# Performance work log

Hardware: AMD Instinct MI355X
Metric: run time of the kernel (lower is better)

## Reference

```python
import jax, jax.numpy as jnp
import numpy as np

B, N, IN_F, OUT_F, H = 4, 1024, 256, 256, 8
HID = OUT_F // H  # 32
ALPHA = 0.2  # leaky relu negative slope


def setup_inputs() -> dict:
    key = jax.random.key(0)
    k1, k2, k3, k4 = jax.random.split(key, 4)
    h = jax.random.normal(k1, (B, N, IN_F), dtype=jnp.float32)
    # linear: in_features -> n_heads*n_hidden, no bias (stored as [in, out])
    W = jax.random.normal(k2, (IN_F, H * HID), dtype=jnp.float32) / np.sqrt(IN_F)
    # attn: Linear(2*n_hidden, 1, bias=False), shared across heads
    attn_w = jax.random.normal(k3, (2 * HID,), dtype=jnp.float32) / np.sqrt(2 * HID)
    # random dense adjacency (p=0.5) plus self loops, broadcast over heads
    u = jax.random.uniform(k4, (B, N, N, 1), dtype=jnp.float32)
    adj_mat = jnp.maximum((u < 0.5).astype(jnp.float32), jnp.eye(N, dtype=jnp.float32)[None, :, :, None])
    return {"h": h, "adj_mat": adj_mat, "W": W, "attn_w": attn_w}


def reference(h, adj_mat, W, attn_w):
    # g: [b, n, h, d]
    g = (h @ W).reshape(B, N, H, HID)
    # attn(concat(g_i, g_j)) decomposes: e[b,i,j,h] = <attn_w[:HID], g_i> + <attn_w[HID:], g_j>
    # (exactly the math of the repeat/repeat_interleave/cat + 1-wide linear, without the N^2 concat)
    e_i = jnp.einsum('bnhd,d->bnh', g, attn_w[:HID])   # g_repeat_interleave part (index i)
    e_j = jnp.einsum('bnhd,d->bnh', g, attn_w[HID:])   # g_repeat part (index j)
    e = e_i[:, :, None, :] + e_j[:, None, :, :]        # [b, i, j, h]
    e = jnp.where(e >= 0, e, ALPHA * e)                # LeakyReLU(alpha)
    e = jnp.where(adj_mat == 0, -jnp.inf, e)           # masked_fill
    a = jax.nn.softmax(e, axis=1)                      # faithful: original uses Softmax(dim=1)
    # dropout p acts as identity in eval mode / p=0
    out = jnp.einsum('bijh,bjhd->bihd', a, g)          # [b, i, h, d]
    return out.reshape(B, N, H * HID)                  # is_concat=True
```

## Files before the change

kernel.cpp:

```cpp
#include <hip/hip_runtime.h>
#include <math.h>

#define BB 4
#define NN 1024
#define HH 8
#define NROW (BB*NN)

typedef short s8v __attribute__((ext_vector_type(8)));
typedef float f4v __attribute__((ext_vector_type(4)));

__device__ __forceinline__ float lrelu(float x) { return fmaxf(x, 0.2f * x); }
__device__ __forceinline__ short bf16rne(float f) {
    unsigned u = __float_as_uint(f);
    u += 0x7FFF + ((u >> 16) & 1u);
    return (short)(u >> 16);
}

__global__ __launch_bounds__(256) void k_gemm_ei(const float* __restrict__ hm,
                                                 const float* __restrict__ W,
                                                 const float* __restrict__ aw,
                                                 float* __restrict__ g,
                                                 float* __restrict__ e_i,
                                                 float* __restrict__ e_j,
                                                 float* __restrict__ e_jt) {
    __shared__ __align__(16) float hs[8][256];
    __shared__ float aws[64];
    const int row0 = blockIdx.x * 8;
    const int t = threadIdx.x;
    if (t < 64) aws[t] = aw[t];
    const float4* h4 = (const float4*)(hm + row0 * 256);
    float4* hs4 = (float4*)&hs[0][0];
    hs4[t] = h4[t];
    hs4[t + 256] = h4[t + 256];
    __syncthreads();

    float c0 = 0.f, c1 = 0.f, c2 = 0.f, c3 = 0.f, c4 = 0.f, c5 = 0.f, c6 = 0.f, c7 = 0.f;
    for (int k4 = 0; k4 < 64; ++k4) {
        const float w0 = W[(4 * k4 + 0) * 256 + t];
        const float w1 = W[(4 * k4 + 1) * 256 + t];
        const float w2 = W[(4 * k4 + 2) * 256 + t];
        const float w3 = W[(4 * k4 + 3) * 256 + t];
#define ROW(r)                                                        \
        {                                                             \
            const float4 hv = *(const float4*)&hs[r][4 * k4];         \
            c##r = fmaf(hv.x, w0, c##r);                              \
            c##r = fmaf(hv.y, w1, c##r);                              \
            c##r = fmaf(hv.z, w2, c##r);                              \
            c##r = fmaf(hv.w, w3, c##r);                              \
        }
        ROW(0) ROW(1) ROW(2) ROW(3) ROW(4) ROW(5) ROW(6) ROW(7)
#undef ROW
    }
    const int d = t & 31, hh = t >> 5;
    const int b = row0 >> 10;
#define EPI(r)                                                                  \
    {                                                                           \
        g[(row0 + r) * 256 + t] = c##r;                                         \
        float vi = c##r * aws[d];                                               \
        float vj = c##r * aws[32 + d];                                          \
        for (int mm = 1; mm < 32; mm <<= 1) {                                   \
            vi += __shfl_xor(vi, mm);                                           \
            vj += __shfl_xor(vj, mm);                                           \
        }                                                                       \
        if (d == 0) {                                                           \
            e_i[(row0 + r) * 8 + hh] = vi;                                      \
            e_j[(row0 + r) * 8 + hh] = vj;                                      \
            e_jt[(size_t)(b * 8 + hh) * NN + ((row0 + r) & (NN - 1))] = vj;     \
        }                                                                       \
    }
    EPI(0) EPI(1) EPI(2) EPI(3) EPI(4) EPI(5) EPI(6) EPI(7)
#undef EPI
}

__global__ __launch_bounds__(256) void k_s(const float* __restrict__ adj,
                                           const float* __restrict__ e_i,
                                           const float* __restrict__ e_j,
                                           float* __restrict__ ps,
                                           unsigned long long* __restrict__ bits) {
    __shared__ __align__(16) float eis[128 * 8];
    __shared__ float ejs[8][64];
    __shared__ float sp[4][8][64];
    const int bx = blockIdx.x;
    const int b = bx >> 7, jc = (bx >> 3) & 15, ic = bx & 7;
    const int j0 = jc * 64, i0 = ic * 128;
    const int t = threadIdx.x;

    ((float4*)eis)[t] = ((const float4*)(e_i + (b * NN + i0) * 8))[t];
    if (t < 128) {
        const float4 v = ((const float4*)(e_j + (b * NN + j0) * 8))[t];
        const int base = t * 4;
        ejs[(base + 0) & 7][(base + 0) >> 3] = v.x;
        ejs[(base + 1) & 7][(base + 1) >> 3] = v.y;
        ejs[(base + 2) & 7][(base + 2) >> 3] = v.z;
        ejs[(base + 3) & 7][(base + 3) >> 3] = v.w;
    }
    __syncthreads();

    const int ii = t >> 6, jj = t & 63;
    const float e0 = ejs[0][jj], e1 = ejs[1][jj], e2 = ejs[2][jj], e3 = ejs[3][jj];
    const float e4 = ejs[4][jj], e5 = ejs[5][jj], e6 = ejs[6][jj], e7 = ejs[7][jj];
    float s0 = 0.f, s1 = 0.f, s2 = 0.f, s3 = 0.f, s4 = 0.f, s5 = 0.f, s6 = 0.f, s7 = 0.f;
    const float* adjp = adj + (size_t)b * NN * NN + j0 + jj;
    for (int i = ii; i < 128; i += 4) {
        const float a = adjp[(size_t)(i0 + i) * NN];
        const unsigned long long mk = __ballot(a != 0.f);
        if (jj == 0) bits[(size_t)(b * NN + i0 + i) * 16 + jc] = mk;
        const f4v eA = *(const f4v*)&eis[i * 8];
        const f4v eB = *(const f4v*)&eis[i * 8 + 4];
        s0 = fmaf(a, __expf(lrelu(eA[0] + e0)), s0);
        s1 = fmaf(a, __expf(lrelu(eA[1] + e1)), s1);
        s2 = fmaf(a, __expf(lrelu(eA[2] + e2)), s2);
        s3 = fmaf(a, __expf(lrelu(eA[3] + e3)), s3);
        s4 = fmaf(a, __expf(lrelu(eB[0] + e4)), s4);
        s5 = fmaf(a, __expf(lrelu(eB[1] + e5)), s5);
        s6 = fmaf(a, __expf(lrelu(eB[2] + e6)), s6);
        s7 = fmaf(a, __expf(lrelu(eB[3] + e7)), s7);
    }
    sp[ii][0][jj] = s0; sp[ii][1][jj] = s1; sp[ii][2][jj] = s2; sp[ii][3][jj] = s3;
    sp[ii][4][jj] = s4; sp[ii][5][jj] = s5; sp[ii][6][jj] = s6; sp[ii][7][jj] = s7;
    __syncthreads();
#pragma unroll
    for (int k = 0; k < 2; ++k) {
        const int idx = t * 2 + k;
        const int jjo = idx >> 3, h = idx & 7;
        const float s = sp[0][h][jjo] + sp[1][h][jjo] + sp[2][h][jjo] + sp[3][h][jjo];
        ps[ic * (NROW * 8) + (b * NN + j0 + jjo) * 8 + h] = s;
    }
}

__global__ __launch_bounds__(256) void k_prep(const float* __restrict__ ps,
                                              const float* __restrict__ g,
                                              short* __restrict__ Gt) {
    __shared__ float rss[16][8];
    const int bx = blockIdx.x;
    const int b = bx >> 6, j0 = (bx & 63) * 16;
    const int t = threadIdx.x;
    if (t < 128) {
        const int jj = t >> 3, h = t & 7;
        float s = 0.f;
#pragma unroll
        for (int ic = 0; ic < 8; ++ic)
            s += ps[ic * (NROW * 8) + (b * NN + j0 + jj) * 8 + h];
        rss[jj][h] = 1.0f / s;
    }
    __syncthreads();
    const int h = t >> 5, d = t & 31;
    uint4 w0, w1;
#define PK(dst, r0, r1)                                                          \
    {                                                                            \
        const float va = g[(size_t)(b * NN + j0 + r0) * 256 + t] * rss[r0][h];   \
        const float vb = g[(size_t)(b * NN + j0 + r1) * 256 + t] * rss[r1][h];   \
        dst = (unsigned)(unsigned short)bf16rne(va) |                            \
              ((unsigned)(unsigned short)bf16rne(vb) << 16);                     \
    }
    PK(w0.x, 0, 1) PK(w0.y, 2, 3) PK(w0.z, 4, 5) PK(w0.w, 6, 7)
    PK(w1.x, 8, 9) PK(w1.y, 10, 11) PK(w1.z, 12, 13) PK(w1.w, 14, 15)
#undef PK
    const int jt = j0 >> 5, jj0 = j0 & 31;
    short* dst = Gt + ((size_t)((b * 8 + h) * 32 + jt)) * 1024 + d * 32 + jj0;
    *(uint4*)dst = w0;
    *(uint4*)(dst + 8) = w1;
}

__global__ __launch_bounds__(256) void k_out_mfma(const unsigned long long* __restrict__ bits,
                                                  const short* __restrict__ Gt,
                                                  const float* __restrict__ e_i,
                                                  const float* __restrict__ e_jt,
                                                  float* __restrict__ out) {
    __shared__ short gts[4][4][32][40];
    __shared__ float ejt[4][128];
    const int bx = blockIdx.x;
    const int hs = bx >> 8, b = (bx >> 6) & 3, i0 = (bx & 63) * 16;
    const int t = threadIdx.x;
    const int wave = t >> 6, lane = t & 63;
    const int m = lane & 15, q = lane >> 4;
    const int h = hs * 4 + wave;

    const float ei = e_i[(size_t)(b * NN + i0 + m) * 8 + h];
    f4v acc0 = {0.f, 0.f, 0.f, 0.f}, acc1 = {0.f, 0.f, 0.f, 0.f};

    const unsigned long long* bitsrow = bits + (size_t)(b * NN + i0 + m) * 16;
    const float4* gtg4 = (const float4*)Gt;
    const float4* ejt4 = (const float4*)(e_jt + (size_t)b * 8 * NN);

    for (int s = 0; s < 8; ++s) {
        float4 g0, g1, g2, g3, g4, g5, g6, g7;
#define LG(k)                                                                     \
        {                                                                         \
            const int u = t + 256 * (k);                                          \
            g##k = gtg4[(size_t)(b * 8 + hs * 4 + (u >> 9)) * 4096 + s * 512 +    \
                        (u & 511)];                                               \
        }
        LG(0) LG(1) LG(2) LG(3) LG(4) LG(5) LG(6) LG(7)
#undef LG
        const ulonglong2 bv = *(const ulonglong2*)&bitsrow[s * 2];
        float4 ev = make_float4(0.f, 0.f, 0.f, 0.f);
        if (t < 128) ev = ejt4[(size_t)(hs * 4 + (t >> 5)) * 256 + s * 32 + (t & 31)];
        __syncthreads();
#define SG(k)                                                                     \
        {                                                                         \
            const int u = t + 256 * (k);                                          \
            char* dstp = (char*)gts + (u >> 9) * 10240 + ((u >> 7) & 3) * 2560 +  \
                         ((u >> 2) & 31) * 80 + (u & 3) * 16;                     \
            *(float4*)dstp = g##k;                                                \
        }
        SG(0) SG(1) SG(2) SG(3) SG(4) SG(5) SG(6) SG(7)
#undef SG
        if (t < 128) *(float4*)&ejt[t >> 5][(t & 31) * 4] = ev;
        __syncthreads();

        const unsigned bw0 = (unsigned)bv.x, bw1 = (unsigned)(bv.x >> 32);
        const unsigned bw2 = (unsigned)bv.y, bw3 = (unsigned)(bv.y >> 32);

#define LT(lt, bw)                                                                \
        {                                                                         \
            const f4v ej0 = *(const f4v*)&ejt[wave][(lt) * 32 + q * 8];           \
            const f4v ej1 = *(const f4v*)&ejt[wave][(lt) * 32 + q * 8 + 4];       \
            s8v A;                                                                \
            A[0] = ((bw >> (q * 8 + 0)) & 1u) ? bf16rne(__expf(lrelu(ei + ej0[0]))) : (short)0; \
            A[1] = ((bw >> (q * 8 + 1)) & 1u) ? bf16rne(__expf(lrelu(ei + ej0[1]))) : (short)0; \
            A[2] = ((bw >> (q * 8 + 2)) & 1u) ? bf16rne(__expf(lrelu(ei + ej0[2]))) : (short)0; \
            A[3] = ((bw >> (q * 8 + 3)) & 1u) ? bf16rne(__expf(lrelu(ei + ej0[3]))) : (short)0; \
            A[4] = ((bw >> (q * 8 + 4)) & 1u) ? bf16rne(__expf(lrelu(ei + ej1[0]))) : (short)0; \
            A[5] = ((bw >> (q * 8 + 5)) & 1u) ? bf16rne(__expf(lrelu(ei + ej1[1]))) : (short)0; \
            A[6] = ((bw >> (q * 8 + 6)) & 1u) ? bf16rne(__expf(lrelu(ei + ej1[2]))) : (short)0; \
            A[7] = ((bw >> (q * 8 + 7)) & 1u) ? bf16rne(__expf(lrelu(ei + ej1[3]))) : (short)0; \
            const s8v B0 = *(const s8v*)&gts[wave][lt][m][q * 8];                 \
            const s8v B1 = *(const s8v*)&gts[wave][lt][m + 16][q * 8];            \
            acc0 = __builtin_amdgcn_mfma_f32_16x16x32_bf16(A, B0, acc0, 0, 0, 0); \
            acc1 = __builtin_amdgcn_mfma_f32_16x16x32_bf16(A, B1, acc1, 0, 0, 0); \
        }
        LT(0, bw0) LT(1, bw1) LT(2, bw2) LT(3, bw3)
#undef LT
    }

    float* op = out + (size_t)(b * NN + i0) * 256;
#pragma unroll
    for (int r = 0; r < 4; ++r) {
        const int row = q * 4 + r;
        op[(size_t)row * 256 + h * 32 + m] = acc0[r];
        op[(size_t)row * 256 + h * 32 + 16 + m] = acc1[r];
    }
}

extern "C" void kernel_launch(void* const* d_in, const int* in_sizes, int n_in,
                              void* d_out, int out_size, void* d_ws, size_t ws_size,
                              hipStream_t stream) {
    const float* h      = (const float*)d_in[0];
    const float* adj    = (const float*)d_in[1];
    const float* W      = (const float*)d_in[2];
    const float* attn_w = (const float*)d_in[3];
    float* out = (float*)d_out;

    float* ws = (float*)d_ws;
    float* g    = ws;
    float* e_i  = g + NROW * 256;
    float* e_j  = e_i + NROW * 8;
    float* e_jt = e_j + NROW * 8;
    float* ps   = e_jt + NROW * 8;
    short* Gt   = (short*)(ps + 8 * NROW * 8);
    unsigned long long* bits = (unsigned long long*)(Gt + 2 * 1048576);

    k_gemm_ei<<<NROW / 8, 256, 0, stream>>>(h, W, attn_w, g, e_i, e_j, e_jt);
    k_s<<<512, 256, 0, stream>>>(adj, e_i, e_j, ps, bits);
    k_prep<<<256, 256, 0, stream>>>(ps, g, Gt);
    k_out_mfma<<<512, 256, 0, stream>>>(bits, Gt, e_i, e_jt, out);
}
```

Before: 129.2 us.

## Split output kernel over j halves with atomic accumulation and use exp2

The final MFMA kernel now splits the j (neighbor) dimension into two halves, doubling the grid to 1024 blocks and accumulating partial results into the output with float atomicAdd after zeroing it with a memset. Separately, the attention logits are prescaled by log2(e) so the exponentials can use the hardware exp2 instruction instead of __expf. The split is meant to add parallelism and occupancy for a kernel whose grid was about two blocks per CU. The cost is an extra memset, atomic traffic on the output, and nondeterministic summation order.

```diff
diff --git a/kernel.cpp b/kernel.cpp
--- a/kernel.cpp
+++ b/kernel.cpp
@@ -5,11 +5,13 @@
 #define NN 1024
 #define HH 8
 #define NROW (BB*NN)
+#define L2E 1.4426950408889634f
 
 typedef short s8v __attribute__((ext_vector_type(8)));
 typedef float f4v __attribute__((ext_vector_type(4)));
 
 __device__ __forceinline__ float lrelu(float x) { return fmaxf(x, 0.2f * x); }
+__device__ __forceinline__ float fexp2(float x) { return __builtin_amdgcn_exp2f(x); }
 __device__ __forceinline__ short bf16rne(float f) {
     unsigned u = __float_as_uint(f);
     u += 0x7FFF + ((u >> 16) & 1u);
@@ -63,9 +65,9 @@
             vj += __shfl_xor(vj, mm);                                           \
         }                                                                       \
         if (d == 0) {                                                           \
-            e_i[(row0 + r) * 8 + hh] = vi;                                      \
-            e_j[(row0 + r) * 8 + hh] = vj;                                      \
-            e_jt[(size_t)(b * 8 + hh) * NN + ((row0 + r) & (NN - 1))] = vj;     \
+            e_i[(row0 + r) * 8 + hh] = vi * L2E;                                \
+            e_j[(row0 + r) * 8 + hh] = vj * L2E;                                \
+            e_jt[(size_t)(b * 8 + hh) * NN + ((row0 + r) & (NN - 1))] = vj * L2E; \
         }                                                                       \
     }
     EPI(0) EPI(1) EPI(2) EPI(3) EPI(4) EPI(5) EPI(6) EPI(7)
@@ -107,14 +109,14 @@
         if (jj == 0) bits[(size_t)(b * NN + i0 + i) * 16 + jc] = mk;
         const f4v eA = *(const f4v*)&eis[i * 8];
         const f4v eB = *(const f4v*)&eis[i * 8 + 4];
-        s0 = fmaf(a, __expf(lrelu(eA[0] + e0)), s0);
-        s1 = fmaf(a, __expf(lrelu(eA[1] + e1)), s1);
-        s2 = fmaf(a, __expf(lrelu(eA[2] + e2)), s2);
-        s3 = fmaf(a, __expf(lrelu(eA[3] + e3)), s3);
-        s4 = fmaf(a, __expf(lrelu(eB[0] + e4)), s4);
-        s5 = fmaf(a, __expf(lrelu(eB[1] + e5)), s5);
-        s6 = fmaf(a, __expf(lrelu(eB[2] + e6)), s6);
-        s7 = fmaf(a, __expf(lrelu(eB[3] + e7)), s7);
+        s0 = fmaf(a, fexp2(lrelu(eA[0] + e0)), s0);
+        s1 = fmaf(a, fexp2(lrelu(eA[1] + e1)), s1);
+        s2 = fmaf(a, fexp2(lrelu(eA[2] + e2)), s2);
+        s3 = fmaf(a, fexp2(lrelu(eA[3] + e3)), s3);
+        s4 = fmaf(a, fexp2(lrelu(eB[0] + e4)), s4);
+        s5 = fmaf(a, fexp2(lrelu(eB[1] + e5)), s5);
+        s6 = fmaf(a, fexp2(lrelu(eB[2] + e6)), s6);
+        s7 = fmaf(a, fexp2(lrelu(eB[3] + e7)), s7);
     }
     sp[ii][0][jj] = s0; sp[ii][1][jj] = s1; sp[ii][2][jj] = s2; sp[ii][3][jj] = s3;
     sp[ii][4][jj] = s4; sp[ii][5][jj] = s5; sp[ii][6][jj] = s6; sp[ii][7][jj] = s7;
@@ -167,10 +169,10 @@
                                                   const float* __restrict__ e_i,
                                                   const float* __restrict__ e_jt,
                                                   float* __restrict__ out) {
-    __shared__ short gts[4][4][32][40];
-    __shared__ float ejt[4][128];
+    __shared__ short gts[4][2][32][40];
+    __shared__ float ejt[4][64];
     const int bx = blockIdx.x;
-    const int hs = bx >> 8, b = (bx >> 6) & 3, i0 = (bx & 63) * 16;
+    const int jhalf = bx >> 9, hs = (bx >> 8) & 1, b = (bx >> 6) & 3, i0 = (bx & 63) * 16;
     const int t = threadIdx.x;
     const int wave = t >> 6, lane = t & 63;
     const int m = lane & 15, q = lane >> 4;
@@ -179,58 +181,58 @@
     const float ei = e_i[(size_t)(b * NN + i0 + m) * 8 + h];
     f4v acc0 = {0.f, 0.f, 0.f, 0.f}, acc1 = {0.f, 0.f, 0.f, 0.f};
 
-    const unsigned long long* bitsrow = bits + (size_t)(b * NN + i0 + m) * 16;
+    const unsigned long long* bitsrow = bits + (size_t)(b * NN + i0 + m) * 16 + jhalf * 8;
     const float4* gtg4 = (const float4*)Gt;
     const float4* ejt4 = (const float4*)(e_jt + (size_t)b * 8 * NN);
 
     for (int s = 0; s < 8; ++s) {
-        float4 g0, g1, g2, g3, g4, g5, g6, g7;
+        float4 g0, g1, g2, g3;
 #define LG(k)                                                                     \
         {                                                                         \
             const int u = t + 256 * (k);                                          \
-            g##k = gtg4[(size_t)(b * 8 + hs * 4 + (u >> 9)) * 4096 + s * 512 +    \
-                        (u & 511)];                                               \
-        }
-        LG(0) LG(1) LG(2) LG(3) LG(4) LG(5) LG(6) LG(7)
+            g##k = gtg4[(size_t)(b * 8 + hs * 4 + (u >> 8)) * 4096 +              \
+                        (jhalf * 16 + s * 2) * 128 + (u & 255)];                  \
+        }
+        LG(0) LG(1) LG(2) LG(3)
 #undef LG
-        const ulonglong2 bv = *(const ulonglong2*)&bitsrow[s * 2];
+        const unsigned long long bv = bitsrow[s];
         float4 ev = make_float4(0.f, 0.f, 0.f, 0.f);
-        if (t < 128) ev = ejt4[(size_t)(hs * 4 + (t >> 5)) * 256 + s * 32 + (t & 31)];
+        if (t < 64)
+            ev = ejt4[(size_t)(hs * 4 + (t >> 4)) * 256 + jhalf * 128 + s * 16 + (t & 15)];
         __syncthreads();
 #define SG(k)                                                                     \
         {                                                                         \
             const int u = t + 256 * (k);                                          \
-            char* dstp = (char*)gts + (u >> 9) * 10240 + ((u >> 7) & 3) * 2560 +  \
+            char* dstp = (char*)gts + (u >> 7) * 2560 +                           \
                          ((u >> 2) & 31) * 80 + (u & 3) * 16;                     \
             *(float4*)dstp = g##k;                                                \
         }
-        SG(0) SG(1) SG(2) SG(3) SG(4) SG(5) SG(6) SG(7)
+        SG(0) SG(1) SG(2) SG(3)
 #undef SG
-        if (t < 128) *(float4*)&ejt[t >> 5][(t & 31) * 4] = ev;
+        if (t < 64) *(float4*)&ejt[t >> 4][(t & 15) * 4] = ev;
         __syncthreads();
 
-        const unsigned bw0 = (unsigned)bv.x, bw1 = (unsigned)(bv.x >> 32);
-        const unsigned bw2 = (unsigned)bv.y, bw3 = (unsigned)(bv.y >> 32);
+        const unsigned bw0 = (unsigned)bv, bw1 = (unsigned)(bv >> 32);
 
 #define LT(lt, bw)                                                                \
         {                                                                         \
             const f4v ej0 = *(const f4v*)&ejt[wave][(lt) * 32 + q * 8];           \
             const f4v ej1 = *(const f4v*)&ejt[wave][(lt) * 32 + q * 8 + 4];       \
             s8v A;                                                                \
-            A[0] = ((bw >> (q * 8 + 0)) & 1u) ? bf16rne(__expf(lrelu(ei + ej0[0]))) : (short)0; \
-            A[1] = ((bw >> (q * 8 + 1)) & 1u) ? bf16rne(__expf(lrelu(ei + ej0[1]))) : (short)0; \
-            A[2] = ((bw >> (q * 8 + 2)) & 1u) ? bf16rne(__expf(lrelu(ei + ej0[2]))) : (short)0; \
-            A[3] = ((bw >> (q * 8 + 3)) & 1u) ? bf16rne(__expf(lrelu(ei + ej0[3]))) : (short)0; \
-            A[4] = ((bw >> (q * 8 + 4)) & 1u) ? bf16rne(__expf(lrelu(ei + ej1[0]))) : (short)0; \
-            A[5] = ((bw >> (q * 8 + 5)) & 1u) ? bf16rne(__expf(lrelu(ei + ej1[1]))) : (short)0; \
-            A[6] = ((bw >> (q * 8 + 6)) & 1u) ? bf16rne(__expf(lrelu(ei + ej1[2]))) : (short)0; \
-            A[7] = ((bw >> (q * 8 + 7)) & 1u) ? bf16rne(__expf(lrelu(ei + ej1[3]))) : (short)0; \
+            A[0] = ((bw >> (q * 8 + 0)) & 1u) ? bf16rne(fexp2(lrelu(ei + ej0[0]))) : (short)0; \
+            A[1] = ((bw >> (q * 8 + 1)) & 1u) ? bf16rne(fexp2(lrelu(ei + ej0[1]))) : (short)0; \
+            A[2] = ((bw >> (q * 8 + 2)) & 1u) ? bf16rne(fexp2(lrelu(ei + ej0[2]))) : (short)0; \
+            A[3] = ((bw >> (q * 8 + 3)) & 1u) ? bf16rne(fexp2(lrelu(ei + ej0[3]))) : (short)0; \
+            A[4] = ((bw >> (q * 8 + 4)) & 1u) ? bf16rne(fexp2(lrelu(ei + ej1[0]))) : (short)0; \
+            A[5] = ((bw >> (q * 8 + 5)) & 1u) ? bf16rne(fexp2(lrelu(ei + ej1[1]))) : (short)0; \
+            A[6] = ((bw >> (q * 8 + 6)) & 1u) ? bf16rne(fexp2(lrelu(ei + ej1[2]))) : (short)0; \
+            A[7] = ((bw >> (q * 8 + 7)) & 1u) ? bf16rne(fexp2(lrelu(ei + ej1[3]))) : (short)0; \
             const s8v B0 = *(const s8v*)&gts[wave][lt][m][q * 8];                 \
             const s8v B1 = *(const s8v*)&gts[wave][lt][m + 16][q * 8];            \
             acc0 = __builtin_amdgcn_mfma_f32_16x16x32_bf16(A, B0, acc0, 0, 0, 0); \
             acc1 = __builtin_amdgcn_mfma_f32_16x16x32_bf16(A, B1, acc1, 0, 0, 0); \
         }
-        LT(0, bw0) LT(1, bw1) LT(2, bw2) LT(3, bw3)
+        LT(0, bw0) LT(1, bw1)
 #undef LT
     }
 
@@ -238,8 +240,8 @@
 #pragma unroll
     for (int r = 0; r < 4; ++r) {
         const int row = q * 4 + r;
-        op[(size_t)row * 256 + h * 32 + m] = acc0[r];
-        op[(size_t)row * 256 + h * 32 + 16 + m] = acc1[r];
+        atomicAdd(&op[(size_t)row * 256 + h * 32 + m], acc0[r]);
+        atomicAdd(&op[(size_t)row * 256 + h * 32 + 16 + m], acc1[r]);
     }
 }
 
@@ -261,8 +263,9 @@
     short* Gt   = (short*)(ps + 8 * NROW * 8);
     unsigned long long* bits = (unsigned long long*)(Gt + 2 * 1048576);
 
+    hipMemsetAsync(out, 0, (size_t)out_size * sizeof(float), stream);
     k_gemm_ei<<<NROW / 8, 256, 0, stream>>>(h, W, attn_w, g, e_i, e_j, e_jt);
     k_s<<<512, 256, 0, stream>>>(adj, e_i, e_j, ps, bits);
     k_prep<<<256, 256, 0, stream>>>(ps, g, Gt);
-    k_out_mfma<<<512, 256, 0, stream>>>(bits, Gt, e_i, e_jt, out);
-}
+    k_out_mfma<<<1024, 256, 0, stream>>>(bits, Gt, e_i, e_jt, out);
+}
```

New measurement: 127.8 us. About the same (-1.1%).
